# Optimization experiments

Hardware: AMD Instinct MI355X
Metric: run time of the kernel (lower is better)

The kernel has to match this reference:

```python
import jax, jax.numpy as jnp
import numpy as np

EPS = 1e-5
SLOPE = 0.01  # torch LeakyReLU default negative slope


def _bn(h, gamma, beta):
    # BatchNorm1d in training mode: biased batch statistics over the batch dim
    mu = jnp.mean(h, axis=0)
    var = jnp.var(h, axis=0)
    return gamma * (h - mu) * jax.lax.rsqrt(var + EPS) + beta


def _leaky(h):
    return jnp.where(h >= 0, h, SLOPE * h)


def _forward(x, adj, w_gc1, b_gc1, w_gc2, b_gc2, w_gc3, b_gc3,
             w_fc0, b_fc0, g_fc0, be_fc0, w_fc1, b_fc1, g_fc1, be_fc1, w_fc2, b_fc2):
    B, S, Fp1 = x.shape
    F = Fp1 - 1
    N = adj.shape[0]
    # --- scatter: build per-sample node features from first S-1 timesteps ---
    sids = x[:, :S - 1, -2].astype(jnp.int32)                                   # [B,S-1]
    feats = jnp.concatenate([x[:, :S - 1, :-2], x[:, :S - 1, -1:]], axis=-1)    # [B,S-1,F]
    X = jnp.zeros((B, N, F), x.dtype).at[jnp.arange(B)[:, None], sids].set(feats)
    # --- symmetric-normalized adjacency with self loops: D^-1/2 (A+I) D^-1/2 ---
    A = adj + jnp.eye(N, dtype=adj.dtype)
    d = jax.lax.rsqrt(jnp.sum(A, axis=1))
    Ahat = d[:, None] * A * d[None, :]                                          # [N,N]
    # --- fc0 branch on last-timestep features ---
    h0 = _leaky(_bn(x[:, -1, :-2] @ w_fc0 + b_fc0, g_fc0, be_fc0))              # [B,FH]
    # --- 3-layer GCN: relu(Ahat @ X @ W + b) ---
    X = jax.nn.relu(jnp.einsum('mn,bnf->bmf', Ahat, X) @ w_gc1 + b_gc1)
    X = jax.nn.relu(jnp.einsum('mn,bnf->bmf', Ahat, X) @ w_gc2 + b_gc2)
    X = jax.nn.relu(jnp.einsum('mn,bnf->bmf', Ahat, X) @ w_gc3 + b_gc3)         # [B,N,GH]
    # --- gather station-specific rows ---
    sid_last = x[:, -1, -2].astype(jnp.int32)                                   # [B]
    g = X[jnp.arange(B), sid_last]                                              # [B,GH]
    # --- fusion MLP head ---
    h = jnp.concatenate([h0, g], axis=1)
    h = _leaky(_bn(h @ w_fc1 + b_fc1, g_fc1, be_fc1))
    return jax.nn.sigmoid(h @ w_fc2 + b_fc2)                                    # [B,1]


def setup_inputs() -> dict:
    B, N, S, F = 128, 2000, 64, 16
    GH, FH = 512, 512
    key = jax.random.key(0)
    ks = jax.random.split(key, 12)
    x = jax.random.normal(ks[0], (B, S, F + 1), dtype=jnp.float32)
    # station-id column (-2): unique ids per sample so scatter writes are unambiguous
    perms = jax.vmap(lambda k: jax.random.permutation(k, N)[:S])(jax.random.split(ks[1], B))  # [B,S]
    x = x.at[:, :, -2].set(perms.astype(jnp.float32))
    # random symmetric 0/1 adjacency, avg degree ~32
    adj = (jax.random.uniform(ks[2], (N, N)) < (32.0 / N)).astype(jnp.float32)
    adj = jnp.maximum(adj, adj.T)

    def lin(k, i, o):
        kw, kb = jax.random.split(k)
        bound = 1.0 / np.sqrt(i)
        w = jax.random.uniform(kw, (i, o), jnp.float32, -bound, bound)
        b = jax.random.uniform(kb, (o,), jnp.float32, -bound, bound)
        return w, b

    w_gc1, b_gc1 = lin(ks[3], F, GH // 2)
    w_gc2, b_gc2 = lin(ks[4], GH // 2, GH // 2)
    w_gc3, b_gc3 = lin(ks[5], GH // 2, GH)
    w_fc0, b_fc0 = lin(ks[6], F - 1, FH)
    w_fc1, b_fc1 = lin(ks[7], GH + FH, FH)
    w_fc2, b_fc2 = lin(ks[8], FH, 1)
    g_fc0 = jnp.ones((FH,), jnp.float32)
    be_fc0 = jnp.zeros((FH,), jnp.float32)
    g_fc1 = jnp.ones((FH,), jnp.float32)
    be_fc1 = jnp.zeros((FH,), jnp.float32)
    return dict(x=x, adj=adj, w_gc1=w_gc1, b_gc1=b_gc1, w_gc2=w_gc2, b_gc2=b_gc2,
                w_gc3=w_gc3, b_gc3=b_gc3, w_fc0=w_fc0, b_fc0=b_fc0, g_fc0=g_fc0, be_fc0=be_fc0,
                w_fc1=w_fc1, b_fc1=b_fc1, g_fc1=g_fc1, be_fc1=be_fc1, w_fc2=w_fc2, b_fc2=b_fc2)


def reference(x, adj, w_gc1, b_gc1, w_gc2, b_gc2, w_gc3, b_gc3, w_fc0, b_fc0, g_fc0, be_fc0,
              w_fc1, b_fc1, g_fc1, be_fc1, w_fc2, b_fc2):
    return _forward(x, adj, w_gc1, b_gc1, w_gc2, b_gc2, w_gc3, b_gc3,
                    w_fc0, b_fc0, g_fc0, be_fc0, w_fc1, b_fc1, g_fc1, be_fc1, w_fc2, b_fc2)
```

## Files before the change

### kernel.cpp

```cpp
#include <hip/hip_runtime.h>
#include <hip/hip_bf16.h>

typedef __hip_bfloat16 bf16;
typedef short s8v __attribute__((ext_vector_type(8)));
typedef float f4v __attribute__((ext_vector_type(4)));
typedef float f2v __attribute__((ext_vector_type(2)));

#define B   128
#define N   2000
#define S   64
#define CAP 128
#define JT  16
#define JG  8
#define XROW 1088

__device__ inline ushort bfb(float v) {
    union { __hip_bfloat16 h; ushort u; } c; c.h = __float2bfloat16(v); return c.u;
}

__global__ __launch_bounds__(256) void k_rowsum(const float* __restrict__ adj,
                                                float* __restrict__ d) {
    int m = blockIdx.x;
    const float* row = adj + (size_t)m * N;
    float s = 0.f;
    for (int c = threadIdx.x; c < N; c += 256) s += row[c];
    for (int o = 32; o > 0; o >>= 1) s += __shfl_down(s, o);
    __shared__ float red[4];
    int wave = threadIdx.x >> 6;
    if ((threadIdx.x & 63) == 0) red[wave] = s;
    __syncthreads();
    if (threadIdx.x == 0)
        d[m] = rsqrtf(red[0] + red[1] + red[2] + red[3] + 1.0f);
}

__global__ __launch_bounds__(64) void k_csr(const float* __restrict__ adj,
                                            const float* __restrict__ d,
                                            int* __restrict__ cnt,
                                            int* __restrict__ idx,
                                            float* __restrict__ val) {
    int m = blockIdx.x;
    int lane = threadIdx.x;
    const float* row = adj + (size_t)m * N;
    float dm = d[m];
    int base = 0;
    for (int c0 = 0; c0 < N; c0 += 64) {
        int c = c0 + lane;
        float a = 0.f;
        if (c < N) { a = row[c]; if (c == m) a += 1.0f; }
        bool pred = (a != 0.f);
        unsigned long long mask = __ballot(pred);
        int pos = base + __popcll(mask & ((1ull << lane) - 1ull));
        if (pred && pos < CAP) {
            idx[m * CAP + pos] = c;
            val[m * CAP + pos] = dm * d[c] * a;
        }
        base += (int)__popcll(mask);
    }
    if (lane == 0) cnt[m] = base < CAP ? base : CAP;
}

__global__ __launch_bounds__(256) void k_extract(const float* __restrict__ x,
                                                 const float* __restrict__ d,
                                                 int* __restrict__ sid,
                                                 int* __restrict__ sid_last,
                                                 uint4* __restrict__ feA) {
    int b = blockIdx.x, tid = threadIdx.x;
    const float* xb = x + (size_t)b * XROW;
    __shared__ float dss_sh[63];
    __shared__ float fe_sh[64][16];
    if (tid < S - 1) {
        int s_ = (int)xb[tid * 17 + 15];
        sid[b * (S - 1) + tid] = s_;
        dss_sh[tid] = d[s_];
    }
    if (tid == S - 1) sid_last[b] = (int)xb[(S - 1) * 17 + 15];
    if (tid >= 240 && tid < 256) fe_sh[63][tid - 240] = 0.f;
    __syncthreads();
    for (int i = tid; i < (S - 1) * 16; i += 256) {
        int t = i >> 4, f = i & 15;
        fe_sh[t][f] = dss_sh[t] * xb[t * 17 + (f < 15 ? f : 16)];
    }
    __syncthreads();
    if (tid < 128) {
        int kc = tid >> 6, l = tid & 63;
        int f = l & 15, tg = l >> 4;
        ushort h[8];
#pragma unroll
        for (int j = 0; j < 8; ++j)
            h[j] = bfb(fe_sh[kc * 32 + tg * 8 + j][f]);
        uint4 r;
        r.x = h[0] | ((uint)h[1] << 16);
        r.y = h[2] | ((uint)h[3] << 16);
        r.z = h[4] | ((uint)h[5] << 16);
        r.w = h[6] | ((uint)h[7] << 16);
        feA[(b * 2 + kc) * 64 + l] = r;
    }
}

__global__ __launch_bounds__(256) void k_packw(const float* __restrict__ w1,
                                               const float* __restrict__ w2,
                                               uint4* __restrict__ wf1,
                                               uint4* __restrict__ wf2) {
    int blk = blockIdx.x;
    if (blk < 4) {
        int e = blk * 256 + threadIdx.x;
        int ct = e >> 6, l = e & 63;
        int kg = l >> 4, ch = ct * 16 + (l & 15);
        ushort h[8];
#pragma unroll
        for (int j = 0; j < 8; ++j) {
            int f = kg * 8 + j;
            h[j] = (f < 16) ? bfb(w1[f * 256 + ch]) : (ushort)0;
        }
        uint4 r;
        r.x = h[0] | ((uint)h[1] << 16);
        r.y = h[2] | ((uint)h[3] << 16);
        r.z = h[4] | ((uint)h[5] << 16);
        r.w = h[6] | ((uint)h[7] << 16);
        wf1[e] = r;
    } else {
        int e = (blk - 4) * 256 + threadIdx.x;
        int l = e & 63;
        int kc = (e >> 6) & 7;
        int nt = e >> 9;
        int col = l & 15, kg = l >> 4;
        ushort h[8];
#pragma unroll
        for (int i = 0; i < 8; ++i) {
            int k = kc * 32 + kg * 8 + i;
            h[i] = bfb(w2[k * 256 + nt * 16 + col]);
        }
        uint4 r;
        r.x = h[0] | ((uint)h[1] << 16);
        r.y = h[2] | ((uint)h[3] << 16);
        r.z = h[4] | ((uint)h[5] << 16);
        r.w = h[6] | ((uint)h[7] << 16);
        wf2[e] = r;
    }
}

__global__ __launch_bounds__(256) void k_x1(const float* __restrict__ adj,
                                            const float* __restrict__ d,
                                            const int* __restrict__ sid,
                                            const uint4* __restrict__ feA,
                                            const uint4* __restrict__ wfrag,
                                            const float* __restrict__ b1,
                                            unsigned char* __restrict__ X1) {
    __shared__ int sv[64];
    __shared__ __align__(16) ushort Ylds[64][40];
    __shared__ float b1s[256];
    __shared__ __align__(16) uint Xs[4][16][68];
    int b = blockIdx.y, p0 = blockIdx.x * 64, tid = threadIdx.x;
    b1s[tid] = b1[tid];
    if (tid < 63) sv[tid] = sid[b * 63 + tid];
    if (tid == 63) sv[63] = 0;
    __syncthreads();

    int l = tid & 63, wv = tid >> 6;
    int lm = l & 15, lg = l >> 4;
    int pt = p0 + wv * 16;
    int pcol = pt + lm;
    bool pv = (pcol < N);
    int pc = pv ? pcol : 0;

    s8v a1_0 = *(const s8v*)&feA[(b * 2 + 0) * 64 + l];
    s8v a1_1 = *(const s8v*)&feA[(b * 2 + 1) * 64 + l];

    int ss[16];
#pragma unroll
    for (int q = 0; q < 16; ++q)
        ss[q] = sv[(q >> 3) * 32 + lg * 8 + (q & 7)];
    float av[16];
#pragma unroll
    for (int q = 0; q < 16; ++q)
        av[q] = adj[(size_t)ss[q] * N + pc];
#pragma unroll
    for (int q = 0; q < 16; ++q) {
        av[q] = pv ? av[q] : 0.f;
        if (pcol == ss[q]) av[q] += 1.0f;
    }
    ushort h[16];
#pragma unroll
    for (int q = 0; q < 16; ++q) h[q] = bfb(av[q]);
    s8v b1f, b2f;
    {
        uint4 t0, t1;
        t0.x = h[0] | ((uint)h[1] << 16);  t0.y = h[2] | ((uint)h[3] << 16);
        t0.z = h[4] | ((uint)h[5] << 16);  t0.w = h[6] | ((uint)h[7] << 16);
        t1.x = h[8] | ((uint)h[9] << 16);  t1.y = h[10] | ((uint)h[11] << 16);
        t1.z = h[12] | ((uint)h[13] << 16); t1.w = h[14] | ((uint)h[15] << 16);
        b1f = *(s8v*)&t0; b2f = *(s8v*)&t1;
    }
    f4v D1 = (f4v){0.f, 0.f, 0.f, 0.f};
    D1 = __builtin_amdgcn_mfma_f32_16x16x32_bf16(a1_0, b1f, D1, 0, 0, 0);
    D1 = __builtin_amdgcn_mfma_f32_16x16x32_bf16(a1_1, b2f, D1, 0, 0, 0);
    float dp = d[pc] * (pv ? 1.f : 0.f);
    uint2 pk;
    pk.x = bfb(D1[0] * dp) | ((uint)bfb(D1[1] * dp) << 16);
    pk.y = bfb(D1[2] * dp) | ((uint)bfb(D1[3] * dp) << 16);
    *(uint2*)&Ylds[wv * 16 + lm][lg * 4] = pk;
    *(uint2*)&Ylds[wv * 16 + lm][16 + lg * 4] = make_uint2(0u, 0u);
    __syncthreads();

    s8v yf = *(const s8v*)&Ylds[wv * 16 + lm][lg * 8];
    f4v acc2[16];
#pragma unroll
    for (int ct = 0; ct < 16; ++ct) acc2[ct] = (f4v){0.f, 0.f, 0.f, 0.f};
#pragma unroll
    for (int ct = 0; ct < 16; ++ct) {
        s8v wfv = *(const s8v*)&wfrag[ct * 64 + l];
        acc2[ct] = __builtin_amdgcn_mfma_f32_16x16x32_bf16(wfv, yf, acc2[ct], 0, 0, 0);
    }
#pragma unroll
    for (int ct = 0; ct < 16; ++ct) {
        float4 bz = *(float4*)&b1s[ct * 16 + lg * 4];
        float v0 = acc2[ct][0] + bz.x; v0 = v0 > 0.f ? v0 : 0.f;
        float v1 = acc2[ct][1] + bz.y; v1 = v1 > 0.f ? v1 : 0.f;
        float v2 = acc2[ct][2] + bz.z; v2 = v2 > 0.f ? v2 : 0.f;
        float v3 = acc2[ct][3] + bz.w; v3 = v3 > 0.f ? v3 : 0.f;
        uint pk8 = (uint)__builtin_amdgcn_cvt_pk_fp8_f32(v0, v1, 0, false);
        pk8 = (uint)__builtin_amdgcn_cvt_pk_fp8_f32(v2, v3, (int)pk8, true);
        Xs[wv][lm][ct * 4 + lg] = pk8;
    }
    __syncthreads();
    {
        uint4* dstb = (uint4*)((uint*)X1 + ((size_t)b * N + p0 + wv * 16) * 64);
#pragma unroll
        for (int i = 0; i < 4; ++i) {
            int g = l + 64 * i;
            int r = g >> 4, c4 = g & 15;
            if (p0 + wv * 16 + r < N)
                dstb[g] = *(uint4*)&Xs[wv][r][c4 * 4];
        }
    }
}

__global__ __launch_bounds__(256) void k_gather(const int* __restrict__ cnt,
                                                const int* __restrict__ idxA,
                                                const float* __restrict__ valA,
                                                const int* __restrict__ sid_last,
                                                const unsigned char* __restrict__ X1,
                                                bf16* __restrict__ aggG) {
    __shared__ int   nns[JG];
    __shared__ int   ncn_s[JG];
    __shared__ int   nidx[JG][CAP];
    __shared__ float nval[JG][CAP];
    int b = blockIdx.y, j0 = blockIdx.x * JG, tid = threadIdx.x;
    int m = sid_last[b];
    int cj = cnt[m];
    if (tid < JG) {
        int j = j0 + tid;
        int n = idxA[m * CAP + (j < cj ? j : 0)];
        nns[tid] = n;
        ncn_s[tid] = (j < cj) ? cnt[n] : 0;
    }
    __syncthreads();
    for (int i = tid; i < JG * CAP; i += 256) {
        int jj = i >> 7, k = i & (CAP - 1);
        int n = nns[jj], c = ncn_s[jj];
        nidx[jj][k] = (k < c) ? idxA[n * CAP + k] : 0;
        nval[jj][k] = (k < c) ? valA[n * CAP + k] : 0.f;
    }
    __syncthreads();
    int lane = tid & 63;
    int w = __builtin_amdgcn_readfirstlane(tid >> 6);
    int la = w * 2, lb = la + 1;
    const uint* X1bl = (const uint*)X1 + (size_t)b * N * 64 + lane;
    int cA = ncn_s[la], cB = ncn_s[lb];
    int cmax = cA > cB ? cA : cB;
    float aA0 = 0.f, aA1 = 0.f, aA2 = 0.f, aA3 = 0.f;
    float aB0 = 0.f, aB1 = 0.f, aB2 = 0.f, aB3 = 0.f;
    if (cmax > 0) {
        uint uA = X1bl[(size_t)nidx[la][0] * 64]; float vA = nval[la][0];
        uint uB = X1bl[(size_t)nidx[lb][0] * 64]; float vB = nval[lb][0];
        for (int k = 0; k < cmax; ++k) {
            uint cuA = uA, cuB = uB;
            float cvA = vA, cvB = vB;
            int kn = (k + 1 < CAP) ? k + 1 : CAP - 1;
            uA = X1bl[(size_t)nidx[la][kn] * 64]; vA = nval[la][kn];
            uB = X1bl[(size_t)nidx[lb][kn] * 64]; vB = nval[lb][kn];
            f2v loA = __builtin_amdgcn_cvt_pk_f32_fp8((int)cuA, false);
            f2v hiA = __builtin_amdgcn_cvt_pk_f32_fp8((int)cuA, true);
            f2v loB = __builtin_amdgcn_cvt_pk_f32_fp8((int)cuB, false);
            f2v hiB = __builtin_amdgcn_cvt_pk_f32_fp8((int)cuB, true);
            aA0 += cvA * loA.x; aA1 += cvA * loA.y;
            aA2 += cvA * hiA.x; aA3 += cvA * hiA.y;
            aB0 += cvB * loB.x; aB1 += cvB * loB.y;
            aB2 += cvB * hiB.x; aB3 += cvB * hiB.y;
        }
    }
    uint2 pkA, pkB;
    pkA.x = bfb(aA0) | ((uint)bfb(aA1) << 16);
    pkA.y = bfb(aA2) | ((uint)bfb(aA3) << 16);
    pkB.x = bfb(aB0) | ((uint)bfb(aB1) << 16);
    pkB.y = bfb(aB2) | ((uint)bfb(aB3) << 16);
    uint2* ag = (uint2*)aggG;
    ag[((size_t)b * CAP + j0 + la) * 64 + lane] = pkA;
    ag[((size_t)b * CAP + j0 + lb) * 64 + lane] = pkB;
}

__global__ __launch_bounds__(256) void k_x2mm(const int* __restrict__ cnt,
                                              const int* __restrict__ sid_last,
                                              const bf16* __restrict__ aggG,
                                              const uint4* __restrict__ w2f,
                                              const float* __restrict__ b2,
                                              float* __restrict__ X2) {
    __shared__ ushort agg[JT][264];
    int b = blockIdx.y, j0 = blockIdx.x * JT, tid = threadIdx.x;
    int m = sid_last[b];
    int cj = cnt[m];
    if (j0 >= cj) return;
    int nj = cj - j0; if (nj > JT) nj = JT;
    {
        const uint4* src = (const uint4*)(aggG + ((size_t)b * CAP + j0) * 256);
        for (int i = tid; i < 512; i += 256) {
            int row = i >> 5, col = i & 31;
            *(uint4*)&agg[row][col * 8] = src[i];
        }
    }
    __syncthreads();
    int lane = tid & 63;
    int w = __builtin_amdgcn_readfirstlane(tid >> 6);
    int col = lane & 15, rg = lane >> 4;
    s8v af[8];
#pragma unroll
    for (int kc = 0; kc < 8; ++kc)
        af[kc] = *(const s8v*)&agg[col][kc * 32 + rg * 8];
#pragma unroll
    for (int t = 0; t < 4; ++t) {
        int nt = w * 4 + t;
        f4v acc = (f4v){0.f, 0.f, 0.f, 0.f};
#pragma unroll
        for (int kc = 0; kc < 8; ++kc) {
            s8v bf = *(const s8v*)&w2f[(nt * 8 + kc) * 64 + lane];
            acc = __builtin_amdgcn_mfma_f32_16x16x32_bf16(af[kc], bf, acc, 0, 0, 0);
        }
        float bv = b2[nt * 16 + col];
        float* dst = X2 + ((size_t)b * CAP + j0) * 256 + nt * 16 + col;
#pragma unroll
        for (int i = 0; i < 4; ++i) {
            int row = rg * 4 + i;
            if (row < nj) {
                float vv = acc[i] + bv;
                dst[(size_t)row * 256] = vv > 0.f ? vv : 0.f;
            }
        }
    }
}

__global__ __launch_bounds__(256) void k_gagg(const int* __restrict__ cnt,
                                              const float* __restrict__ valA,
                                              const int* __restrict__ sid_last,
                                              const float* __restrict__ X2,
                                              float* __restrict__ gagg) {
    int b = blockIdx.x, tid = threadIdx.x;
    int m = sid_last[b];
    int cj = cnt[m];
    const float* vp = valA + m * CAP;
    const float* xp = X2 + (size_t)b * CAP * 256 + tid;
    float a0 = 0.f, a1 = 0.f, a2 = 0.f, a3 = 0.f;
    int jj = 0;
    for (; jj + 4 <= cj; jj += 4) {
        a0 += vp[jj]     * xp[(size_t)(jj)     * 256];
        a1 += vp[jj + 1] * xp[(size_t)(jj + 1) * 256];
        a2 += vp[jj + 2] * xp[(size_t)(jj + 2) * 256];
        a3 += vp[jj + 3] * xp[(size_t)(jj + 3) * 256];
    }
    for (; jj < cj; ++jj) a0 += vp[jj] * xp[(size_t)jj * 256];
    gagg[b * 256 + tid] = (a0 + a1) + (a2 + a3);
}

__global__ __launch_bounds__(256) void k_gmm(const float* __restrict__ gagg,
                                             const float* __restrict__ w3,
                                             const float* __restrict__ b3,
                                             float* __restrict__ g) {
    int b = blockIdx.x, ot = blockIdx.y, tid = threadIdx.x;
    __shared__ float h[256];
    h[tid] = gagg[b * 256 + tid];
    __syncthreads();
    int q  = tid & 31;
    int kg = tid >> 5;
    const float4* w4 = (const float4*)w3;
    int wq = ot * 32 + q;
    float4 acc = {0.f, 0.f, 0.f, 0.f};
    for (int k = kg * 32; k < kg * 32 + 32; ++k) {
        float hk = h[k];
        float4 w = w4[(size_t)k * 128 + wq];
        acc.x += hk * w.x; acc.y += hk * w.y; acc.z += hk * w.z; acc.w += hk * w.w;
    }
    __shared__ float4 red[8][32];
    red[kg][q] = acc;
    __syncthreads();
    if (tid < 32) {
        float4 s = red[0][tid];
#pragma unroll
        for (int gr = 1; gr < 8; ++gr) {
            float4 r = red[gr][tid];
            s.x += r.x; s.y += r.y; s.z += r.z; s.w += r.w;
        }
        int ob = ot * 128 + tid * 4;
        s.x += b3[ob];     s.x = s.x > 0.f ? s.x : 0.f;
        s.y += b3[ob + 1]; s.y = s.y > 0.f ? s.y : 0.f;
        s.z += b3[ob + 2]; s.z = s.z > 0.f ? s.z : 0.f;
        s.w += b3[ob + 3]; s.w = s.w > 0.f ? s.w : 0.f;
        *(float4*)&g[(size_t)b * 512 + ob] = s;
    }
}

__global__ __launch_bounds__(256) void k_fc0(const float* __restrict__ x,
                                             const float* __restrict__ w0,
                                             const float* __restrict__ b0,
                                             float* __restrict__ hp0) {
    int i = blockIdx.x * 256 + threadIdx.x;
    int b = i >> 9, o = i & 511;
    const float* xr = x + (size_t)b * XROW + (S - 1) * 17;
    float acc = b0[o];
#pragma unroll
    for (int f = 0; f < 15; ++f) acc += xr[f] * w0[f * 512 + o];
    hp0[i] = acc;
}

__global__ __launch_bounds__(256) void k_bnstats(const float* __restrict__ h,
                                                 float* __restrict__ mu,
                                                 float* __restrict__ rstd) {
    int o = blockIdx.x * 256 + threadIdx.x;
    float s = 0.f, s2 = 0.f;
    for (int b = 0; b < B; ++b) { float v = h[b * 512 + o]; s += v; s2 += v * v; }
    float m = s * (1.f / B);
    float var = s2 * (1.f / B) - m * m;
    mu[o] = m;
    rstd[o] = rsqrtf(var + 1e-5f);
}

__global__ __launch_bounds__(256) void k_fc1(const float* __restrict__ hp0,
                                             const float* __restrict__ mu0,
                                             const float* __restrict__ rstd0,
                                             const float* __restrict__ gam,
                                             const float* __restrict__ bet,
                                             const float* __restrict__ gbuf,
                                             const float* __restrict__ w1,
                                             const float* __restrict__ b1,
                                             float* __restrict__ hp1) {
    int b = blockIdx.x, ot = blockIdx.y, tid = threadIdx.x;
    __shared__ float h[1024];
    for (int o = tid; o < 512; o += 256) {
        float v = hp0[b * 512 + o];
        v = gam[o] * (v - mu0[o]) * rstd0[o] + bet[o];
        h[o] = v >= 0.f ? v : 0.01f * v;
        h[512 + o] = gbuf[(size_t)b * 512 + o];
    }
    __syncthreads();
    int q  = tid & 31;
    int kg = tid >> 5;
    const float4* w4 = (const float4*)w1;
    int wq = ot * 32 + q;
    float4 acc = {0.f, 0.f, 0.f, 0.f};
    for (int k = kg * 128; k < kg * 128 + 128; ++k) {
        float hk = h[k];
        float4 w = w4[(size_t)k * 128 + wq];
        acc.x += hk * w.x; acc.y += hk * w.y; acc.z += hk * w.z; acc.w += hk * w.w;
    }
    __shared__ float4 red[8][32];
    red[kg][q] = acc;
    __syncthreads();
    if (tid < 32) {
        float4 s = red[0][tid];
#pragma unroll
        for (int gr = 1; gr < 8; ++gr) {
            float4 r = red[gr][tid];
            s.x += r.x; s.y += r.y; s.z += r.z; s.w += r.w;
        }
        int ob = ot * 128 + tid * 4;
        s.x += b1[ob]; s.y += b1[ob + 1]; s.z += b1[ob + 2]; s.w += b1[ob + 3];
        *(float4*)&hp1[b * 512 + ob] = s;
    }
}

__global__ __launch_bounds__(64) void k_out(const float* __restrict__ hp1,
                                            const float* __restrict__ mu1,
                                            const float* __restrict__ rstd1,
                                            const float* __restrict__ gam,
                                            const float* __restrict__ bet,
                                            const float* __restrict__ w2,
                                            const float* __restrict__ b2,
                                            float* __restrict__ out) {
    int b = blockIdx.x, lane = threadIdx.x;
    float acc = 0.f;
    for (int o = lane; o < 512; o += 64) {
        float v = hp1[b * 512 + o];
        v = gam[o] * (v - mu1[o]) * rstd1[o] + bet[o];
        v = v >= 0.f ? v : 0.01f * v;
        acc += v * w2[o];
    }
    for (int off = 32; off > 0; off >>= 1) acc += __shfl_down(acc, off);
    if (lane == 0) out[b] = 1.f / (1.f + expf(-(acc + b2[0])));
}

static inline size_t align256(size_t x) { return (x + 255) & ~(size_t)255; }

extern "C" void kernel_launch(void* const* d_in, const int* in_sizes, int n_in,
                              void* d_out, int out_size, void* d_ws, size_t ws_size,
                              hipStream_t stream) {
    const float* x     = (const float*)d_in[0];
    const float* adj   = (const float*)d_in[1];
    const float* w_gc1 = (const float*)d_in[2];
    const float* b_gc1 = (const float*)d_in[3];
    const float* w_gc2 = (const float*)d_in[4];
    const float* b_gc2 = (const float*)d_in[5];
    const float* w_gc3 = (const float*)d_in[6];
    const float* b_gc3 = (const float*)d_in[7];
    const float* w_fc0 = (const float*)d_in[8];
    const float* b_fc0 = (const float*)d_in[9];
    const float* g_fc0 = (const float*)d_in[10];
    const float* be_fc0= (const float*)d_in[11];
    const float* w_fc1 = (const float*)d_in[12];
    const float* b_fc1 = (const float*)d_in[13];
    const float* g_fc1 = (const float*)d_in[14];
    const float* be_fc1= (const float*)d_in[15];
    const float* w_fc2 = (const float*)d_in[16];
    const float* b_fc2 = (const float*)d_in[17];

    char* wsp = (char*)d_ws;
    size_t off = 0;
    auto alloc = [&](size_t bytes) { void* p = wsp + off; off = align256(off + bytes); return p; };
    float* d_deg   = (float*)alloc((size_t)N * 4);
    int*   sid     = (int*)  alloc((size_t)B * 63 * 4);
    int*   sidl    = (int*)  alloc((size_t)B * 4);
    uint4* feA     = (uint4*)alloc((size_t)B * 2 * 64 * 16);
    uint4* wfrag   = (uint4*)alloc((size_t)1024 * 16);
    uint4* w2frag  = (uint4*)alloc((size_t)8192 * 16);
    int*   csr_cnt = (int*)  alloc((size_t)N * 4);
    int*   csr_idx = (int*)  alloc((size_t)N * CAP * 4);
    float* csr_val = (float*)alloc((size_t)N * CAP * 4);
    unsigned char* X1 = (unsigned char*)alloc((size_t)B * N * 256);
    bf16*  aggG    = (bf16*) alloc((size_t)B * CAP * 256 * 2);
    float* X2      = (float*)alloc((size_t)B * CAP * 256 * 4);
    float* gagg    = (float*)alloc((size_t)B * 256 * 4);
    float* gbuf    = (float*)alloc((size_t)B * 512 * 4);
    float* hp0     = (float*)alloc((size_t)B * 512 * 4);
    float* mu0     = (float*)alloc(512 * 4);
    float* rstd0   = (float*)alloc(512 * 4);
    float* hp1     = (float*)alloc((size_t)B * 512 * 4);
    float* mu1     = (float*)alloc(512 * 4);
    float* rstd1   = (float*)alloc(512 * 4);

    k_rowsum <<<N, 256, 0, stream>>>(adj, d_deg);
    k_csr    <<<N, 64, 0, stream>>>(adj, d_deg, csr_cnt, csr_idx, csr_val);
    k_packw  <<<36, 256, 0, stream>>>(w_gc1, w_gc2, wfrag, w2frag);
    k_extract<<<B, 256, 0, stream>>>(x, d_deg, sid, sidl, feA);
    k_x1     <<<dim3(32, B), 256, 0, stream>>>(adj, d_deg, sid, feA, wfrag, b_gc1, X1);
    k_gather <<<dim3(CAP / JG, B), 256, 0, stream>>>(csr_cnt, csr_idx, csr_val, sidl, X1, aggG);
    k_x2mm   <<<dim3(CAP / JT, B), 256, 0, stream>>>(csr_cnt, sidl, aggG, w2frag, b_gc2, X2);
    k_gagg   <<<B, 256, 0, stream>>>(csr_cnt, csr_val, sidl, X2, gagg);
    k_gmm    <<<dim3(B, 4), 256, 0, stream>>>(gagg, w_gc3, b_gc3, gbuf);
    k_fc0    <<<(B * 512) / 256, 256, 0, stream>>>(x, w_fc0, b_fc0, hp0);
    k_bnstats<<<2, 256, 0, stream>>>(hp0, mu0, rstd0);
    k_fc1    <<<dim3(B, 4), 256, 0, stream>>>(hp0, mu0, rstd0, g_fc0, be_fc0, gbuf, w_fc1, b_fc1, hp1);
    k_bnstats<<<2, 256, 0, stream>>>(hp1, mu1, rstd1);
    k_out    <<<B, 64, 0, stream>>>(hp1, mu1, rstd1, g_fc1, be_fc1, w_fc2, b_fc2, (float*)d_out);
}
```

Before: 145.1 us.

## Merge prep kernels, unroll gather by two, split gagg, fuse fc0 with BN stats

Measured after the change: 134.7 us. 7.1% less time.

```diff
diff --git a/kernel.cpp b/kernel.cpp
--- a/kernel.cpp
+++ b/kernel.cpp
@@ -18,124 +18,127 @@
     union { __hip_bfloat16 h; ushort u; } c; c.h = __float2bfloat16(v); return c.u;
 }
 
-__global__ __launch_bounds__(256) void k_rowsum(const float* __restrict__ adj,
-                                                float* __restrict__ d) {
-    int m = blockIdx.x;
-    const float* row = adj + (size_t)m * N;
-    float s = 0.f;
-    for (int c = threadIdx.x; c < N; c += 256) s += row[c];
-    for (int o = 32; o > 0; o >>= 1) s += __shfl_down(s, o);
-    __shared__ float red[4];
-    int wave = threadIdx.x >> 6;
-    if ((threadIdx.x & 63) == 0) red[wave] = s;
-    __syncthreads();
-    if (threadIdx.x == 0)
-        d[m] = rsqrtf(red[0] + red[1] + red[2] + red[3] + 1.0f);
-}
-
-__global__ __launch_bounds__(64) void k_csr(const float* __restrict__ adj,
-                                            const float* __restrict__ d,
-                                            int* __restrict__ cnt,
-                                            int* __restrict__ idx,
-                                            float* __restrict__ val) {
-    int m = blockIdx.x;
-    int lane = threadIdx.x;
-    const float* row = adj + (size_t)m * N;
-    float dm = d[m];
-    int base = 0;
-    for (int c0 = 0; c0 < N; c0 += 64) {
-        int c = c0 + lane;
-        float a = 0.f;
-        if (c < N) { a = row[c]; if (c == m) a += 1.0f; }
-        bool pred = (a != 0.f);
-        unsigned long long mask = __ballot(pred);
-        int pos = base + __popcll(mask & ((1ull << lane) - 1ull));
-        if (pred && pos < CAP) {
-            idx[m * CAP + pos] = c;
-            val[m * CAP + pos] = dm * d[c] * a;
-        }
-        base += (int)__popcll(mask);
-    }
-    if (lane == 0) cnt[m] = base < CAP ? base : CAP;
-}
-
-__global__ __launch_bounds__(256) void k_extract(const float* __restrict__ x,
-                                                 const float* __restrict__ d,
-                                                 int* __restrict__ sid,
-                                                 int* __restrict__ sid_last,
-                                                 uint4* __restrict__ feA) {
-    int b = blockIdx.x, tid = threadIdx.x;
-    const float* xb = x + (size_t)b * XROW;
-    __shared__ float dss_sh[63];
-    __shared__ float fe_sh[64][16];
-    if (tid < S - 1) {
-        int s_ = (int)xb[tid * 17 + 15];
-        sid[b * (S - 1) + tid] = s_;
-        dss_sh[tid] = d[s_];
-    }
-    if (tid == S - 1) sid_last[b] = (int)xb[(S - 1) * 17 + 15];
-    if (tid >= 240 && tid < 256) fe_sh[63][tid - 240] = 0.f;
-    __syncthreads();
-    for (int i = tid; i < (S - 1) * 16; i += 256) {
-        int t = i >> 4, f = i & 15;
-        fe_sh[t][f] = dss_sh[t] * xb[t * 17 + (f < 15 ? f : 16)];
-    }
-    __syncthreads();
-    if (tid < 128) {
-        int kc = tid >> 6, l = tid & 63;
-        int f = l & 15, tg = l >> 4;
-        ushort h[8];
-#pragma unroll
-        for (int j = 0; j < 8; ++j)
-            h[j] = bfb(fe_sh[kc * 32 + tg * 8 + j][f]);
-        uint4 r;
-        r.x = h[0] | ((uint)h[1] << 16);
-        r.y = h[2] | ((uint)h[3] << 16);
-        r.z = h[4] | ((uint)h[5] << 16);
-        r.w = h[6] | ((uint)h[7] << 16);
-        feA[(b * 2 + kc) * 64 + l] = r;
-    }
-}
-
-__global__ __launch_bounds__(256) void k_packw(const float* __restrict__ w1,
+__global__ __launch_bounds__(256) void k_prep0(const float* __restrict__ adj,
+                                               float* __restrict__ d,
+                                               const float* __restrict__ w1,
                                                const float* __restrict__ w2,
                                                uint4* __restrict__ wf1,
                                                uint4* __restrict__ wf2) {
     int blk = blockIdx.x;
-    if (blk < 4) {
-        int e = blk * 256 + threadIdx.x;
-        int ct = e >> 6, l = e & 63;
-        int kg = l >> 4, ch = ct * 16 + (l & 15);
-        ushort h[8];
-#pragma unroll
-        for (int j = 0; j < 8; ++j) {
-            int f = kg * 8 + j;
-            h[j] = (f < 16) ? bfb(w1[f * 256 + ch]) : (ushort)0;
-        }
-        uint4 r;
-        r.x = h[0] | ((uint)h[1] << 16);
-        r.y = h[2] | ((uint)h[3] << 16);
-        r.z = h[4] | ((uint)h[5] << 16);
-        r.w = h[6] | ((uint)h[7] << 16);
-        wf1[e] = r;
+    if (blk < N) {
+        int m = blk;
+        const float* row = adj + (size_t)m * N;
+        float s = 0.f;
+        for (int c = threadIdx.x; c < N; c += 256) s += row[c];
+        for (int o = 32; o > 0; o >>= 1) s += __shfl_down(s, o);
+        __shared__ float red[4];
+        int wave = threadIdx.x >> 6;
+        if ((threadIdx.x & 63) == 0) red[wave] = s;
+        __syncthreads();
+        if (threadIdx.x == 0)
+            d[m] = rsqrtf(red[0] + red[1] + red[2] + red[3] + 1.0f);
     } else {
-        int e = (blk - 4) * 256 + threadIdx.x;
-        int l = e & 63;
-        int kc = (e >> 6) & 7;
-        int nt = e >> 9;
-        int col = l & 15, kg = l >> 4;
-        ushort h[8];
-#pragma unroll
-        for (int i = 0; i < 8; ++i) {
-            int k = kc * 32 + kg * 8 + i;
-            h[i] = bfb(w2[k * 256 + nt * 16 + col]);
-        }
-        uint4 r;
-        r.x = h[0] | ((uint)h[1] << 16);
-        r.y = h[2] | ((uint)h[3] << 16);
-        r.z = h[4] | ((uint)h[5] << 16);
-        r.w = h[6] | ((uint)h[7] << 16);
-        wf2[e] = r;
+        int blk2 = blk - N;
+        if (blk2 < 4) {
+            int e = blk2 * 256 + threadIdx.x;
+            int ct = e >> 6, l = e & 63;
+            int kg = l >> 4, ch = ct * 16 + (l & 15);
+            ushort h[8];
+#pragma unroll
+            for (int j = 0; j < 8; ++j) {
+                int f = kg * 8 + j;
+                h[j] = (f < 16) ? bfb(w1[f * 256 + ch]) : (ushort)0;
+            }
+            uint4 r;
+            r.x = h[0] | ((uint)h[1] << 16);
+            r.y = h[2] | ((uint)h[3] << 16);
+            r.z = h[4] | ((uint)h[5] << 16);
+            r.w = h[6] | ((uint)h[7] << 16);
+            wf1[e] = r;
+        } else {
+            int e = (blk2 - 4) * 256 + threadIdx.x;
+            int l = e & 63;
+            int kc = (e >> 6) & 7;
+            int nt = e >> 9;
+            int col = l & 15, kg = l >> 4;
+            ushort h[8];
+#pragma unroll
+            for (int i = 0; i < 8; ++i) {
+                int k = kc * 32 + kg * 8 + i;
+                h[i] = bfb(w2[k * 256 + nt * 16 + col]);
+            }
+            uint4 r;
+            r.x = h[0] | ((uint)h[1] << 16);
+            r.y = h[2] | ((uint)h[3] << 16);
+            r.z = h[4] | ((uint)h[5] << 16);
+            r.w = h[6] | ((uint)h[7] << 16);
+            wf2[e] = r;
+        }
+    }
+}
+
+__global__ __launch_bounds__(256) void k_prep1(const float* __restrict__ adj,
+                                               const float* __restrict__ d,
+                                               const float* __restrict__ x,
+                                               int* __restrict__ cnt,
+                                               int* __restrict__ idx,
+                                               float* __restrict__ val,
+                                               int* __restrict__ sid,
+                                               int* __restrict__ sid_last,
+                                               uint4* __restrict__ feA) {
+    int blk = blockIdx.x;
+    if (blk < 500) {
+        int m = blk * 4 + (threadIdx.x >> 6);
+        int lane = threadIdx.x & 63;
+        const float* row = adj + (size_t)m * N;
+        float dm = d[m];
+        int base = 0;
+        for (int c0 = 0; c0 < N; c0 += 64) {
+            int c = c0 + lane;
+            float a = 0.f;
+            if (c < N) { a = row[c]; if (c == m) a += 1.0f; }
+            bool pred = (a != 0.f);
+            unsigned long long mask = __ballot(pred);
+            int pos = base + __popcll(mask & ((1ull << lane) - 1ull));
+            if (pred && pos < CAP) {
+                idx[m * CAP + pos] = c;
+                val[m * CAP + pos] = dm * d[c] * a;
+            }
+            base += (int)__popcll(mask);
+        }
+        if (lane == 0) cnt[m] = base < CAP ? base : CAP;
+    } else {
+        int b = blk - 500, tid = threadIdx.x;
+        const float* xb = x + (size_t)b * XROW;
+        __shared__ float dss_sh[63];
+        __shared__ float fe_sh[64][16];
+        if (tid < S - 1) {
+            int s_ = (int)xb[tid * 17 + 15];
+            sid[b * (S - 1) + tid] = s_;
+            dss_sh[tid] = d[s_];
+        }
+        if (tid == S - 1) sid_last[b] = (int)xb[(S - 1) * 17 + 15];
+        if (tid >= 240 && tid < 256) fe_sh[63][tid - 240] = 0.f;
+        __syncthreads();
+        for (int i = tid; i < (S - 1) * 16; i += 256) {
+            int t = i >> 4, f = i & 15;
+            fe_sh[t][f] = dss_sh[t] * xb[t * 17 + (f < 15 ? f : 16)];
+        }
+        __syncthreads();
+        if (tid < 128) {
+            int kc = tid >> 6, l = tid & 63;
+            int f = l & 15, tg = l >> 4;
+            ushort h[8];
+#pragma unroll
+            for (int j = 0; j < 8; ++j)
+                h[j] = bfb(fe_sh[kc * 32 + tg * 8 + j][f]);
+            uint4 r;
+            r.x = h[0] | ((uint)h[1] << 16);
+            r.y = h[2] | ((uint)h[3] << 16);
+            r.z = h[4] | ((uint)h[5] << 16);
+            r.w = h[6] | ((uint)h[7] << 16);
+            feA[(b * 2 + kc) * 64 + l] = r;
+        }
     }
 }
 
@@ -271,22 +274,33 @@
     float aA0 = 0.f, aA1 = 0.f, aA2 = 0.f, aA3 = 0.f;
     float aB0 = 0.f, aB1 = 0.f, aB2 = 0.f, aB3 = 0.f;
     if (cmax > 0) {
-        uint uA = X1bl[(size_t)nidx[la][0] * 64]; float vA = nval[la][0];
-        uint uB = X1bl[(size_t)nidx[lb][0] * 64]; float vB = nval[lb][0];
-        for (int k = 0; k < cmax; ++k) {
-            uint cuA = uA, cuB = uB;
-            float cvA = vA, cvB = vB;
-            int kn = (k + 1 < CAP) ? k + 1 : CAP - 1;
-            uA = X1bl[(size_t)nidx[la][kn] * 64]; vA = nval[la][kn];
-            uB = X1bl[(size_t)nidx[lb][kn] * 64]; vB = nval[lb][kn];
-            f2v loA = __builtin_amdgcn_cvt_pk_f32_fp8((int)cuA, false);
-            f2v hiA = __builtin_amdgcn_cvt_pk_f32_fp8((int)cuA, true);
-            f2v loB = __builtin_amdgcn_cvt_pk_f32_fp8((int)cuB, false);
-            f2v hiB = __builtin_amdgcn_cvt_pk_f32_fp8((int)cuB, true);
-            aA0 += cvA * loA.x; aA1 += cvA * loA.y;
-            aA2 += cvA * hiA.x; aA3 += cvA * hiA.y;
-            aB0 += cvB * loB.x; aB1 += cvB * loB.y;
-            aB2 += cvB * hiB.x; aB3 += cvB * hiB.y;
+        uint uA0 = X1bl[(size_t)nidx[la][0] * 64]; float vA0 = nval[la][0];
+        uint uA1 = X1bl[(size_t)nidx[la][1] * 64]; float vA1 = nval[la][1];
+        uint uB0 = X1bl[(size_t)nidx[lb][0] * 64]; float vB0 = nval[lb][0];
+        uint uB1 = X1bl[(size_t)nidx[lb][1] * 64]; float vB1 = nval[lb][1];
+        int c2 = (cmax + 1) & ~1;
+        for (int k = 0; k < c2; k += 2) {
+            int k2 = k + 2; k2 = k2 < CAP ? k2 : CAP - 1;
+            int k3 = k + 3; k3 = k3 < CAP ? k3 : CAP - 1;
+            uint cA0 = uA0, cA1 = uA1, cB0 = uB0, cB1 = uB1;
+            float wA0 = vA0, wA1 = vA1, wB0 = vB0, wB1 = vB1;
+            uA0 = X1bl[(size_t)nidx[la][k2] * 64]; vA0 = nval[la][k2];
+            uA1 = X1bl[(size_t)nidx[la][k3] * 64]; vA1 = nval[la][k3];
+            uB0 = X1bl[(size_t)nidx[lb][k2] * 64]; vB0 = nval[lb][k2];
+            uB1 = X1bl[(size_t)nidx[lb][k3] * 64]; vB1 = nval[lb][k3];
+            f2v lo, hi;
+            lo = __builtin_amdgcn_cvt_pk_f32_fp8((int)cA0, false);
+            hi = __builtin_amdgcn_cvt_pk_f32_fp8((int)cA0, true);
+            aA0 += wA0 * lo.x; aA1 += wA0 * lo.y; aA2 += wA0 * hi.x; aA3 += wA0 * hi.y;
+            lo = __builtin_amdgcn_cvt_pk_f32_fp8((int)cA1, false);
+            hi = __builtin_amdgcn_cvt_pk_f32_fp8((int)cA1, true);
+            aA0 += wA1 * lo.x; aA1 += wA1 * lo.y; aA2 += wA1 * hi.x; aA3 += wA1 * hi.y;
+            lo = __builtin_amdgcn_cvt_pk_f32_fp8((int)cB0, false);
+            hi = __builtin_amdgcn_cvt_pk_f32_fp8((int)cB0, true);
+            aB0 += wB0 * lo.x; aB1 += wB0 * lo.y; aB2 += wB0 * hi.x; aB3 += wB0 * hi.y;
+            lo = __builtin_amdgcn_cvt_pk_f32_fp8((int)cB1, false);
+            hi = __builtin_amdgcn_cvt_pk_f32_fp8((int)cB1, true);
+            aB0 += wB1 * lo.x; aB1 += wB1 * lo.y; aB2 += wB1 * hi.x; aB3 += wB1 * hi.y;
         }
     }
     uint2 pkA, pkB;
@@ -352,31 +366,35 @@
                                               const float* __restrict__ valA,
                                               const int* __restrict__ sid_last,
                                               const float* __restrict__ X2,
-                                              float* __restrict__ gagg) {
-    int b = blockIdx.x, tid = threadIdx.x;
+                                              float* __restrict__ gaggP) {
+    int b = blockIdx.x, q = blockIdx.y, tid = threadIdx.x;
     int m = sid_last[b];
     int cj = cnt[m];
+    int jlo = q * 32, jhi = jlo + 32 < cj ? jlo + 32 : cj;
     const float* vp = valA + m * CAP;
     const float* xp = X2 + (size_t)b * CAP * 256 + tid;
     float a0 = 0.f, a1 = 0.f, a2 = 0.f, a3 = 0.f;
-    int jj = 0;
-    for (; jj + 4 <= cj; jj += 4) {
+    int jj = jlo;
+    for (; jj + 4 <= jhi; jj += 4) {
         a0 += vp[jj]     * xp[(size_t)(jj)     * 256];
         a1 += vp[jj + 1] * xp[(size_t)(jj + 1) * 256];
         a2 += vp[jj + 2] * xp[(size_t)(jj + 2) * 256];
         a3 += vp[jj + 3] * xp[(size_t)(jj + 3) * 256];
     }
-    for (; jj < cj; ++jj) a0 += vp[jj] * xp[(size_t)jj * 256];
-    gagg[b * 256 + tid] = (a0 + a1) + (a2 + a3);
-}
-
-__global__ __launch_bounds__(256) void k_gmm(const float* __restrict__ gagg,
+    for (; jj < jhi; ++jj) a0 += vp[jj] * xp[(size_t)jj * 256];
+    gaggP[((size_t)b * 4 + q) * 256 + tid] = (a0 + a1) + (a2 + a3);
+}
+
+__global__ __launch_bounds__(256) void k_gmm(const float* __restrict__ gaggP,
                                              const float* __restrict__ w3,
                                              const float* __restrict__ b3,
                                              float* __restrict__ g) {
     int b = blockIdx.x, ot = blockIdx.y, tid = threadIdx.x;
     __shared__ float h[256];
-    h[tid] = gagg[b * 256 + tid];
+    {
+        const float* p = gaggP + (size_t)b * 4 * 256 + tid;
+        h[tid] = p[0] + p[256] + p[512] + p[768];
+    }
     __syncthreads();
     int q  = tid & 31;
     int kg = tid >> 5;
@@ -407,29 +425,62 @@
     }
 }
 
-__global__ __launch_bounds__(256) void k_fc0(const float* __restrict__ x,
-                                             const float* __restrict__ w0,
-                                             const float* __restrict__ b0,
-                                             float* __restrict__ hp0) {
-    int i = blockIdx.x * 256 + threadIdx.x;
-    int b = i >> 9, o = i & 511;
+__global__ __launch_bounds__(256) void k_fc0s(const float* __restrict__ x,
+                                              const float* __restrict__ w0,
+                                              const float* __restrict__ b0,
+                                              float* __restrict__ hp0,
+                                              float* __restrict__ mu0,
+                                              float* __restrict__ rstd0) {
+    int tid = threadIdx.x;
+    int c = tid >> 7, b = tid & 127;
+    int o = blockIdx.x * 2 + c;
     const float* xr = x + (size_t)b * XROW + (S - 1) * 17;
     float acc = b0[o];
 #pragma unroll
     for (int f = 0; f < 15; ++f) acc += xr[f] * w0[f * 512 + o];
-    hp0[i] = acc;
-}
-
-__global__ __launch_bounds__(256) void k_bnstats(const float* __restrict__ h,
-                                                 float* __restrict__ mu,
-                                                 float* __restrict__ rstd) {
-    int o = blockIdx.x * 256 + threadIdx.x;
+    hp0[b * 512 + o] = acc;
+    float s = acc, s2 = acc * acc;
+    for (int off = 32; off > 0; off >>= 1) {
+        s += __shfl_down(s, off);
+        s2 += __shfl_down(s2, off);
+    }
+    __shared__ float rs[4], rs2[4];
+    int wv = tid >> 6;
+    if ((tid & 63) == 0) { rs[wv] = s; rs2[wv] = s2; }
+    __syncthreads();
+    if ((tid & 127) == 0) {
+        float S1 = rs[c * 2] + rs[c * 2 + 1];
+        float S2 = rs2[c * 2] + rs2[c * 2 + 1];
+        float m = S1 * (1.f / B);
+        float var = S2 * (1.f / B) - m * m;
+        mu0[o] = m;
+        rstd0[o] = rsqrtf(var + 1e-5f);
+    }
+}
+
+__global__ __launch_bounds__(256) void k_bn1w(const float* __restrict__ h,
+                                              float* __restrict__ mu,
+                                              float* __restrict__ rstd) {
+    int tid = threadIdx.x;
+    int o = blockIdx.x * 32 + (tid & 31);
+    int bg = tid >> 5;
     float s = 0.f, s2 = 0.f;
-    for (int b = 0; b < B; ++b) { float v = h[b * 512 + o]; s += v; s2 += v * v; }
-    float m = s * (1.f / B);
-    float var = s2 * (1.f / B) - m * m;
-    mu[o] = m;
-    rstd[o] = rsqrtf(var + 1e-5f);
+    for (int b = bg * 16; b < bg * 16 + 16; ++b) {
+        float v = h[b * 512 + o];
+        s += v; s2 += v * v;
+    }
+    __shared__ float rs[8][32], rs2[8][32];
+    rs[bg][tid & 31] = s; rs2[bg][tid & 31] = s2;
+    __syncthreads();
+    if (tid < 32) {
+        float S1 = 0.f, S2 = 0.f;
+#pragma unroll
+        for (int g2 = 0; g2 < 8; ++g2) { S1 += rs[g2][tid]; S2 += rs2[g2][tid]; }
+        float m = S1 * (1.f / B);
+        float var = S2 * (1.f / B) - m * m;
+        mu[blockIdx.x * 32 + tid] = m;
+        rstd[blockIdx.x * 32 + tid] = rsqrtf(var + 1e-5f);
+    }
 }
 
 __global__ __launch_bounds__(256) void k_fc1(const float* __restrict__ hp0,
@@ -535,7 +586,7 @@
     unsigned char* X1 = (unsigned char*)alloc((size_t)B * N * 256);
     bf16*  aggG    = (bf16*) alloc((size_t)B * CAP * 256 * 2);
     float* X2      = (float*)alloc((size_t)B * CAP * 256 * 4);
-    float* gagg    = (float*)alloc((size_t)B * 256 * 4);
+    float* gaggP   = (float*)alloc((size_t)B * 4 * 256 * 4);
     float* gbuf    = (float*)alloc((size_t)B * 512 * 4);
     float* hp0     = (float*)alloc((size_t)B * 512 * 4);
     float* mu0     = (float*)alloc(512 * 4);
@@ -544,18 +595,15 @@
     float* mu1     = (float*)alloc(512 * 4);
     float* rstd1   = (float*)alloc(512 * 4);
 
-    k_rowsum <<<N, 256, 0, stream>>>(adj, d_deg);
-    k_csr    <<<N, 64, 0, stream>>>(adj, d_deg, csr_cnt, csr_idx, csr_val);
-    k_packw  <<<36, 256, 0, stream>>>(w_gc1, w_gc2, wfrag, w2frag);
-    k_extract<<<B, 256, 0, stream>>>(x, d_deg, sid, sidl, feA);
-    k_x1     <<<dim3(32, B), 256, 0, stream>>>(adj, d_deg, sid, feA, wfrag, b_gc1, X1);
-    k_gather <<<dim3(CAP / JG, B), 256, 0, stream>>>(csr_cnt, csr_idx, csr_val, sidl, X1, aggG);
-    k_x2mm   <<<dim3(CAP / JT, B), 256, 0, stream>>>(csr_cnt, sidl, aggG, w2frag, b_gc2, X2);
-    k_gagg   <<<B, 256, 0, stream>>>(csr_cnt, csr_val, sidl, X2, gagg);
-    k_gmm    <<<dim3(B, 4), 256, 0, stream>>>(gagg, w_gc3, b_gc3, gbuf);
-    k_fc0    <<<(B * 512) / 256, 256, 0, stream>>>(x, w_fc0, b_fc0, hp0);
-    k_bnstats<<<2, 256, 0, stream>>>(hp0, mu0, rstd0);
-    k_fc1    <<<dim3(B, 4), 256, 0, stream>>>(hp0, mu0, rstd0, g_fc0, be_fc0, gbuf, w_fc1, b_fc1, hp1);
-    k_bnstats<<<2, 256, 0, stream>>>(hp1, mu1, rstd1);
-    k_out    <<<B, 64, 0, stream>>>(hp1, mu1, rstd1, g_fc1, be_fc1, w_fc2, b_fc2, (float*)d_out);
-}
+    k_prep0 <<<N + 36, 256, 0, stream>>>(adj, d_deg, w_gc1, w_gc2, wfrag, w2frag);
+    k_prep1 <<<500 + B, 256, 0, stream>>>(adj, d_deg, x, csr_cnt, csr_idx, csr_val, sid, sidl, feA);
+    k_x1    <<<dim3(32, B), 256, 0, stream>>>(adj, d_deg, sid, feA, wfrag, b_gc1, X1);
+    k_gather<<<dim3(CAP / JG, B), 256, 0, stream>>>(csr_cnt, csr_idx, csr_val, sidl, X1, aggG);
+    k_x2mm  <<<dim3(CAP / JT, B), 256, 0, stream>>>(csr_cnt, sidl, aggG, w2frag, b_gc2, X2);
+    k_gagg  <<<dim3(B, 4), 256, 0, stream>>>(csr_cnt, csr_val, sidl, X2, gaggP);
+    k_gmm   <<<dim3(B, 4), 256, 0, stream>>>(gaggP, w_gc3, b_gc3, gbuf);
+    k_fc0s  <<<256, 256, 0, stream>>>(x, w_fc0, b_fc0, hp0, mu0, rstd0);
+    k_fc1   <<<dim3(B, 4), 256, 0, stream>>>(hp0, mu0, rstd0, g_fc0, be_fc0, gbuf, w_fc1, b_fc1, hp1);
+    k_bn1w  <<<16, 256, 0, stream>>>(hp1, mu1, rstd1);
+    k_out   <<<B, 64, 0, stream>>>(hp1, mu1, rstd1, g_fc1, be_fc1, w_fc2, b_fc2, (float*)d_out);
+}
```
